# Performance work log

Measured on AMD Instinct MI355X. Metric: run time of the kernel, lower is better.

## Reference

```python
import jax, jax.numpy as jnp
import numpy as np

B, L, H, D = 2, 2048, 8, 64
LOCAL_WINDOW = 32   # init arg
STRIDE = 64         # init arg


def _sparse_mask(L_Q, L_K, dtype):
    # Self-attention branch (L_Q == L_K): union of a local band of half-width
    # local_window//2 and strided diagonals at offsets that are multiples of (stride+1).
    i = jnp.arange(L_Q)[:, None]
    j = jnp.arange(L_K)[None, :]
    d = jnp.abs(i - j)
    band = d <= (LOCAL_WINDOW // 2)
    strided = (d % (STRIDE + 1)) == 0
    return (band | strided).astype(dtype)


def setup_inputs() -> dict:
    key = jax.random.key(0)
    kx, kq, kk, kv = jax.random.split(key, 4)
    x = jax.random.normal(kx, (B, L, H, D), jnp.float32)
    queries = jax.random.normal(kq, (B, L, H, D), jnp.float32)
    keys = jax.random.normal(kk, (B, L, H, D), jnp.float32)
    values = jax.random.normal(kv, (B, L, H, D), jnp.float32)
    # TriangularCausalMask: True on strictly upper triangle -> masked with -inf
    causal = jnp.triu(jnp.ones((L, L), dtype=bool), k=1)
    attn_mask = jnp.broadcast_to(causal[None, None], (B, 1, L, L))
    return {"x": x, "queries": queries, "keys": keys, "values": values,
            "attn_mask": attn_mask}


def reference(x, queries, keys, values, attn_mask):
    Bq, L_Q, Hh, Dh = queries.shape
    L_K = keys.shape[1]
    scale = 1.0 / np.sqrt(Dh)  # self.scale is None
    # [B,H,L_Q,L_K]
    scores = jnp.einsum('blhe,bshe->bhls', queries, keys)
    sparse = _sparse_mask(L_Q, L_K, scores.dtype)  # [L_Q, L_K]
    # NOTE: torch code ZEROES (not -inf) the non-sparse entries, then applies
    # the causal mask with -inf, then softmaxes scale*scores. Faithful here.
    scores = scores * sparse
    scores = jnp.where(attn_mask, -jnp.inf, scores)
    A = jax.nn.softmax(scale * scores, axis=-1)  # dropout = identity (eval)
    V = jnp.einsum('bhls,bshd->blhd', A, values)
    return V
```

## Files before the change

### kernel.cpp

```cpp
#include <hip/hip_runtime.h>

#define Bc 2
#define Lc 2048
#define Hc 8
#define Dc 64
#define TL 16
#define NT (Lc / TL)
#define RHD (Hc * Dc)
#define SP1 65
#define SCALE 0.125f

template <int CTRL>
__device__ __forceinline__ float dpp_add(float x) {
    int p = __builtin_amdgcn_update_dpp(0, __float_as_int(x), CTRL, 0xF, 0xF, true);
    return x + __int_as_float(p);
}
__device__ __forceinline__ float row16_sum(float x) {
    x = dpp_add<0xB1>(x);
    x = dpp_add<0x4E>(x);
    x = dpp_add<0x141>(x);
    x = dpp_add<0x140>(x);
    return x;
}

__global__ __launch_bounds__(256)
void dozer_chunk_sum(const float* __restrict__ V, float* __restrict__ partials) {
    const int bh = blockIdx.x;
    const int t  = blockIdx.y;
    const int b  = bh >> 3;
    const int h  = bh & 7;
    const int g  = threadIdx.x >> 6;
    const int d  = threadIdx.x & 63;
    const float* Vbh = V + (size_t)b * Lc * RHD + h * Dc;
    const int l0 = t * TL;
    float s = 0.f;
    for (int r = g; r < TL; r += 4)
        s += Vbh[(size_t)(l0 + r) * RHD + d];
    __shared__ float red[4][64];
    red[g][d] = s;
    __syncthreads();
    if (g == 0)
        partials[((size_t)bh * NT + t) * 64 + d] =
            red[0][d] + red[1][d] + red[2][d] + red[3][d];
}

__global__ __launch_bounds__(256)
void dozer_main(const float* __restrict__ Q, const float* __restrict__ K,
                const float* __restrict__ V, const float* __restrict__ partials,
                float* __restrict__ out) {
    const int bh   = blockIdx.x;
    const int t    = blockIdx.y;
    const int b    = bh >> 3;
    const int h    = bh & 7;
    const int tid  = threadIdx.x;
    const int wave = tid >> 6;
    const int lane = tid & 63;
    const int l0   = t * TL;

    const float* Qbh = Q + (size_t)b * Lc * RHD + h * Dc;
    const float* Kbh = K + (size_t)b * Lc * RHD + h * Dc;
    const float* Vbh = V + (size_t)b * Lc * RHD + h * Dc;

    __shared__ float Ptile[TL][64];
    __shared__ float red[8][64];

    {
        const int d = lane;
        float pbase = 0.f;
        if (partials) {
            const float* pb = partials + (size_t)bh * NT * 64;
            for (int c = wave; c < t; c += 4)
                pbase += pb[(size_t)c * 64 + d];
        } else {
            for (int s = wave; s < l0; s += 4)
                pbase += Vbh[(size_t)s * RHD + d];
        }
        const float* vr = Vbh + (size_t)(l0 + 4 * wave) * RHD + d;
        const float x0 = vr[0];
        const float x1 = vr[RHD];
        const float x2 = vr[2 * RHD];
        const float x3 = vr[3 * RHD];
        const float s0 = x0, s1 = s0 + x1, s2 = s1 + x2, s3 = s2 + x3;
        red[wave][d]     = pbase;
        red[4 + wave][d] = s3;
        __syncthreads();
        float base = red[0][d] + red[1][d] + red[2][d] + red[3][d];
        if (wave > 0) base += red[4][d];
        if (wave > 1) base += red[5][d];
        if (wave > 2) base += red[6][d];
        Ptile[4 * wave + 0][d] = base + s0;
        Ptile[4 * wave + 1][d] = base + s1;
        Ptile[4 * wave + 2][d] = base + s2;
        Ptile[4 * wave + 3][d] = base + s3;
        __syncthreads();
    }

    const int p  = lane >> 4;
    const int dd = lane & 15;

    for (int rr = 0; rr < 4; ++rr) {
        const int r = wave * 4 + rr;
        const int l = l0 + r;

        float4 q4 = *(const float4*)&Qbh[(size_t)l * RHD + dd * 4];
        q4.x *= SCALE; q4.y *= SCALE; q4.z *= SCALE; q4.w *= SCALE;

        float4 acc = make_float4(0.f, 0.f, 0.f, 0.f);
        float  den = 0.f;

        #pragma unroll
        for (int it = 0; it < 4; ++it) {
            const int pi = p + 4 * it;
            const bool ok = (pi <= l);
            int j = l - pi; if (j < 0) j = 0;
            const float* Kr = Kbh + (size_t)j * RHD + dd * 4;
            const float* Vr = Vbh + (size_t)j * RHD + dd * 4;
            const float4 k4 = *(const float4*)Kr;
            const float4 v4 = *(const float4*)Vr;
            float dot = q4.x * k4.x + q4.y * k4.y + q4.z * k4.z + q4.w * k4.w;
            dot = row16_sum(dot);
            float w = __expf(dot) - 1.f;
            w = ok ? w : 0.f;
            acc.x += w * v4.x; acc.y += w * v4.y;
            acc.z += w * v4.z; acc.w += w * v4.w;
            den += w;
        }

        #pragma unroll 4
        for (int it = 0; it < 8; ++it) {
            const int f   = p + 4 * it;
            int off = SP1 * f; if (off < 16) off = 16;
            const bool ok = (off <= l);
            int j = l - off; if (j < 0) j = 0;
            const float* Kr = Kbh + (size_t)j * RHD + dd * 4;
            const float* Vr = Vbh + (size_t)j * RHD + dd * 4;
            const float4 k4 = *(const float4*)Kr;
            const float4 v4 = *(const float4*)Vr;
            float dot = q4.x * k4.x + q4.y * k4.y + q4.z * k4.z + q4.w * k4.w;
            dot = row16_sum(dot);
            float w = __expf(dot) - 1.f;
            w = ok ? w : 0.f;
            acc.x += w * v4.x; acc.y += w * v4.y;
            acc.z += w * v4.z; acc.w += w * v4.w;
            den += w;
        }

        acc.x += __shfl_xor(acc.x, 16, 64); acc.x += __shfl_xor(acc.x, 32, 64);
        acc.y += __shfl_xor(acc.y, 16, 64); acc.y += __shfl_xor(acc.y, 32, 64);
        acc.z += __shfl_xor(acc.z, 16, 64); acc.z += __shfl_xor(acc.z, 32, 64);
        acc.w += __shfl_xor(acc.w, 16, 64); acc.w += __shfl_xor(acc.w, 32, 64);
        den   += __shfl_xor(den, 16, 64);   den   += __shfl_xor(den, 32, 64);

        const float inv = 1.f / ((float)(l + 1) + den);
        if (p == 0) {
            const float4 P4 = *(const float4*)&Ptile[r][dd * 4];
            float4 o;
            o.x = (P4.x + acc.x) * inv;
            o.y = (P4.y + acc.y) * inv;
            o.z = (P4.z + acc.z) * inv;
            o.w = (P4.w + acc.w) * inv;
            *(float4*)&out[((size_t)(b * Lc + l) * Hc + h) * Dc + dd * 4] = o;
        }
    }
}

extern "C" void kernel_launch(void* const* d_in, const int* in_sizes, int n_in,
                              void* d_out, int out_size, void* d_ws, size_t ws_size,
                              hipStream_t stream) {
    const float* Q = (const float*)d_in[1];
    const float* K = (const float*)d_in[2];
    const float* V = (const float*)d_in[3];
    float* out = (float*)d_out;

    const size_t need = (size_t)Bc * Hc * NT * 64 * sizeof(float);
    float* partials = (ws_size >= need) ? (float*)d_ws : nullptr;

    dim3 grid(Bc * Hc, NT);
    if (partials)
        dozer_chunk_sum<<<grid, 256, 0, stream>>>(V, partials);
    dozer_main<<<grid, 256, 0, stream>>>(Q, K, V, partials, out);
}
```

Measured before the change: 130.2 us.

## Software-pipeline K/V loads, trim strided iterations per row, reverse tile order

The two gather loops (local band and strided diagonals) are merged into one loop whose trip count depends on the row index, so rows near the start skip strided offsets that fall before position zero. The K/V rows for the next iteration are prefetched into registers while the current dot product and exp are computed. Block order along the sequence axis is reversed so the tiles with the longest prefix-partial sums launch first, and the partial-sum loop gets an unroll hint. The merged loop is no longer fully unrolled, which adds loop overhead and register pressure from double buffering.

```diff
diff --git a/kernel.cpp b/kernel.cpp
--- a/kernel.cpp
+++ b/kernel.cpp
@@ -49,7 +49,7 @@
                 const float* __restrict__ V, const float* __restrict__ partials,
                 float* __restrict__ out) {
     const int bh   = blockIdx.x;
-    const int t    = blockIdx.y;
+    const int t    = (NT - 1) - blockIdx.y;
     const int b    = bh >> 3;
     const int h    = bh & 7;
     const int tid  = threadIdx.x;
@@ -69,6 +69,7 @@
         float pbase = 0.f;
         if (partials) {
             const float* pb = partials + (size_t)bh * NT * 64;
+            #pragma unroll 4
             for (int c = wave; c < t; c += 4)
                 pbase += pb[(size_t)c * 64 + d];
         } else {
@@ -101,6 +102,7 @@
     for (int rr = 0; rr < 4; ++rr) {
         const int r = wave * 4 + rr;
         const int l = l0 + r;
+        const int nit = 5 + l / 260;
 
         float4 q4 = *(const float4*)&Qbh[(size_t)l * RHD + dd * 4];
         q4.x *= SCALE; q4.y *= SCALE; q4.z *= SCALE; q4.w *= SCALE;
@@ -108,41 +110,36 @@
         float4 acc = make_float4(0.f, 0.f, 0.f, 0.f);
         float  den = 0.f;
 
-        #pragma unroll
-        for (int it = 0; it < 4; ++it) {
-            const int pi = p + 4 * it;
-            const bool ok = (pi <= l);
-            int j = l - pi; if (j < 0) j = 0;
-            const float* Kr = Kbh + (size_t)j * RHD + dd * 4;
-            const float* Vr = Vbh + (size_t)j * RHD + dd * 4;
-            const float4 k4 = *(const float4*)Kr;
-            const float4 v4 = *(const float4*)Vr;
-            float dot = q4.x * k4.x + q4.y * k4.y + q4.z * k4.z + q4.w * k4.w;
+        bool okc = (p <= l);
+        int  j0  = l - p; if (j0 < 0) j0 = 0;
+        float4 kc = *(const float4*)(Kbh + (size_t)j0 * RHD + dd * 4);
+        float4 vc = *(const float4*)(Vbh + (size_t)j0 * RHD + dd * 4);
+
+        for (int it = 0; it < nit; ++it) {
+            float4 kn = kc, vn = vc;
+            bool okn = false;
+            if (it + 1 < nit) {
+                const int it1 = it + 1;
+                int off;
+                if (it1 < 4) {
+                    off = p + 4 * it1;
+                } else {
+                    off = SP1 * (p + 4 * (it1 - 4));
+                    if (off < 16) off = 16;
+                }
+                okn = (off <= l);
+                int j1 = l - off; if (j1 < 0) j1 = 0;
+                kn = *(const float4*)(Kbh + (size_t)j1 * RHD + dd * 4);
+                vn = *(const float4*)(Vbh + (size_t)j1 * RHD + dd * 4);
+            }
+            float dot = q4.x * kc.x + q4.y * kc.y + q4.z * kc.z + q4.w * kc.w;
             dot = row16_sum(dot);
             float w = __expf(dot) - 1.f;
-            w = ok ? w : 0.f;
-            acc.x += w * v4.x; acc.y += w * v4.y;
-            acc.z += w * v4.z; acc.w += w * v4.w;
+            w = okc ? w : 0.f;
+            acc.x += w * vc.x; acc.y += w * vc.y;
+            acc.z += w * vc.z; acc.w += w * vc.w;
             den += w;
-        }
-
-        #pragma unroll 4
-        for (int it = 0; it < 8; ++it) {
-            const int f   = p + 4 * it;
-            int off = SP1 * f; if (off < 16) off = 16;
-            const bool ok = (off <= l);
-            int j = l - off; if (j < 0) j = 0;
-            const float* Kr = Kbh + (size_t)j * RHD + dd * 4;
-            const float* Vr = Vbh + (size_t)j * RHD + dd * 4;
-            const float4 k4 = *(const float4*)Kr;
-            const float4 v4 = *(const float4*)Vr;
-            float dot = q4.x * k4.x + q4.y * k4.y + q4.z * k4.z + q4.w * k4.w;
-            dot = row16_sum(dot);
-            float w = __expf(dot) - 1.f;
-            w = ok ? w : 0.f;
-            acc.x += w * v4.x; acc.y += w * v4.y;
-            acc.z += w * v4.z; acc.w += w * v4.w;
-            den += w;
+            kc = kn; vc = vn; okc = okn;
         }
 
         acc.x += __shfl_xor(acc.x, 16, 64); acc.x += __shfl_xor(acc.x, 32, 64);
```

Measured after the change: 122.8 us. -5.6%, faster.

## Stage local K/V band in shared memory and pipeline strided far loads

Applied to the files above, without the earlier changes.

The local-window keys and values for each 16-row tile are staged cooperatively into shared memory, so the band terms read from LDS rather than making repeated global loads. The strided far-diagonal loop now runs only over the valid count per row, with double-buffered register prefetch of the K/V rows. Blocks are issued in reverse tile order so the heaviest tiles start first, and the reduction scratch is aliased onto the band buffer. This adds shared-memory use and barriers, and the far loop becomes data-dependent.

```diff
diff --git a/kernel.cpp b/kernel.cpp
--- a/kernel.cpp
+++ b/kernel.cpp
@@ -49,7 +49,7 @@
                 const float* __restrict__ V, const float* __restrict__ partials,
                 float* __restrict__ out) {
     const int bh   = blockIdx.x;
-    const int t    = blockIdx.y;
+    const int t    = (NT - 1) - blockIdx.y;
     const int b    = bh >> 3;
     const int h    = bh & 7;
     const int tid  = threadIdx.x;
@@ -61,14 +61,17 @@
     const float* Kbh = K + (size_t)b * Lc * RHD + h * Dc;
     const float* Vbh = V + (size_t)b * Lc * RHD + h * Dc;
 
+    __shared__ float Kband[32][64];
+    __shared__ float Vband[32][64];
     __shared__ float Ptile[TL][64];
-    __shared__ float red[8][64];
+    float (*red)[64] = (float(*)[64])Kband;
 
     {
         const int d = lane;
         float pbase = 0.f;
         if (partials) {
             const float* pb = partials + (size_t)bh * NT * 64;
+            #pragma unroll 4
             for (int c = wave; c < t; c += 4)
                 pbase += pb[(size_t)c * 64 + d];
         } else {
@@ -95,12 +98,27 @@
         __syncthreads();
     }
 
+    {
+        const int i  = tid >> 4;
+        const int c4 = (tid & 15) * 4;
+        #pragma unroll
+        for (int rnd = 0; rnd < 2; ++rnd) {
+            const int ii = i + 16 * rnd;
+            int j = l0 - 16 + ii; if (j < 0) j = 0;
+            *(float4*)&Kband[ii][c4] = *(const float4*)(Kbh + (size_t)j * RHD + c4);
+            *(float4*)&Vband[ii][c4] = *(const float4*)(Vbh + (size_t)j * RHD + c4);
+        }
+        __syncthreads();
+    }
+
     const int p  = lane >> 4;
     const int dd = lane & 15;
 
     for (int rr = 0; rr < 4; ++rr) {
         const int r = wave * 4 + rr;
         const int l = l0 + r;
+        const int nk   = l / SP1;
+        const int nfar = (nk + 3) >> 2;
 
         float4 q4 = *(const float4*)&Qbh[(size_t)l * RHD + dd * 4];
         q4.x *= SCALE; q4.y *= SCALE; q4.z *= SCALE; q4.w *= SCALE;
@@ -108,15 +126,15 @@
         float4 acc = make_float4(0.f, 0.f, 0.f, 0.f);
         float  den = 0.f;
 
-        #pragma unroll
-        for (int it = 0; it < 4; ++it) {
-            const int pi = p + 4 * it;
-            const bool ok = (pi <= l);
-            int j = l - pi; if (j < 0) j = 0;
-            const float* Kr = Kbh + (size_t)j * RHD + dd * 4;
-            const float* Vr = Vbh + (size_t)j * RHD + dd * 4;
-            const float4 k4 = *(const float4*)Kr;
-            const float4 v4 = *(const float4*)Vr;
+        auto farload = [&](float4& k4, float4& v4, int m) {
+            const int f = 1 + p + 4 * m;
+            int j = l - SP1 * f; if (j < 0) j = 0;
+            k4 = *(const float4*)(Kbh + (size_t)j * RHD + dd * 4);
+            v4 = *(const float4*)(Vbh + (size_t)j * RHD + dd * 4);
+        };
+        auto farstep = [&](const float4& k4, const float4& v4, int m) {
+            const int f = 1 + p + 4 * m;
+            const bool ok = (f <= nk);
             float dot = q4.x * k4.x + q4.y * k4.y + q4.z * k4.z + q4.w * k4.w;
             dot = row16_sum(dot);
             float w = __expf(dot) - 1.f;
@@ -124,18 +142,19 @@
             acc.x += w * v4.x; acc.y += w * v4.y;
             acc.z += w * v4.z; acc.w += w * v4.w;
             den += w;
-        }
-
-        #pragma unroll 4
-        for (int it = 0; it < 8; ++it) {
-            const int f   = p + 4 * it;
-            int off = SP1 * f; if (off < 16) off = 16;
+        };
+
+        float4 kA = make_float4(0.f,0.f,0.f,0.f), vA = kA, kB = kA, vB = kA;
+        if (nfar > 0) farload(kA, vA, 0);
+        if (nfar > 1) farload(kB, vB, 1);
+
+        #pragma unroll
+        for (int it = 0; it < 4; ++it) {
+            const int off = p + 4 * it;
+            const int idx = r + 16 - off;
             const bool ok = (off <= l);
-            int j = l - off; if (j < 0) j = 0;
-            const float* Kr = Kbh + (size_t)j * RHD + dd * 4;
-            const float* Vr = Vbh + (size_t)j * RHD + dd * 4;
-            const float4 k4 = *(const float4*)Kr;
-            const float4 v4 = *(const float4*)Vr;
+            const float4 k4 = *(const float4*)&Kband[idx][dd * 4];
+            const float4 v4 = *(const float4*)&Vband[idx][dd * 4];
             float dot = q4.x * k4.x + q4.y * k4.y + q4.z * k4.z + q4.w * k4.w;
             dot = row16_sum(dot);
             float w = __expf(dot) - 1.f;
@@ -144,6 +163,27 @@
             acc.z += w * v4.z; acc.w += w * v4.w;
             den += w;
         }
+        {
+            const bool ok = (p == 0) && (l >= 16);
+            const float4 k4 = *(const float4*)&Kband[r][dd * 4];
+            const float4 v4 = *(const float4*)&Vband[r][dd * 4];
+            float dot = q4.x * k4.x + q4.y * k4.y + q4.z * k4.z + q4.w * k4.w;
+            dot = row16_sum(dot);
+            float w = __expf(dot) - 1.f;
+            w = ok ? w : 0.f;
+            acc.x += w * v4.x; acc.y += w * v4.y;
+            acc.z += w * v4.z; acc.w += w * v4.w;
+            den += w;
+        }
+
+        int m = 0;
+        for (; m + 1 < nfar; m += 2) {
+            farstep(kA, vA, m);
+            if (m + 2 < nfar) farload(kA, vA, m + 2);
+            farstep(kB, vB, m + 1);
+            if (m + 3 < nfar) farload(kB, vB, m + 3);
+        }
+        if (m < nfar) farstep(kA, vA, m);
 
         acc.x += __shfl_xor(acc.x, 16, 64); acc.x += __shfl_xor(acc.x, 32, 64);
         acc.y += __shfl_xor(acc.y, 16, 64); acc.y += __shfl_xor(acc.y, 32, 64);
```

Result: faster. 115.7 us (-11.2%).
